# Performance work log

Measured on AMD Instinct MI355X. Metric: run time of the kernel, lower is better.

The kernel has to match this reference:

```python
import jax, jax.numpy as jnp
import numpy as np

B, T, D, L, E = 4096, 4, 1024, 2, 4  # batch, tasks (risk_num+1), dim, layers, experts/task


def setup_inputs() -> dict:
    key = jax.random.key(0)
    ks = jax.random.split(key, 9)
    s = 1.0 / np.sqrt(D).astype(np.float32)  # torch Linear-style uniform scale
    se = 1.0 / np.sqrt(E).astype(np.float32)
    u = lambda k, shape, sc: jax.random.uniform(k, shape, jnp.float32, -sc, sc)
    return {
        "x": jax.random.normal(ks[0], (B, T, D), jnp.float32),
        # per-layer, per-task shared-expert MLP params (mlp_level=2)
        "W1": u(ks[1], (L, T, D, D), s), "b1": u(ks[2], (L, T, D), s),
        "W2": u(ks[3], (L, T, D, D), s), "b2": u(ks[4], (L, T, D), s),
        # integration weights over E (aliased) experts per task
        "inte": u(ks[5], (L, T, E), se),
        # one shared gate per layer: Linear(D -> T) + softmax
        "Wg": u(ks[6], (L, D, T), s), "bg": u(ks[7], (L, T), s),
    }


def reference(x, W1, b1, W2, b2, inte, Wg, bg):
    h = x  # [B, T, D]
    n_layers = W1.shape[0]
    for l in range(n_layers):
        # per-task 2-layer MLP expert (all E experts per task share weights in the
        # original due to [MLP]*E aliasing)
        t1 = jax.nn.relu(jnp.einsum('btd,tdo->bto', h, W1[l]) + b1[l])
        t2 = jax.nn.relu(jnp.einsum('btd,tdo->bto', t1, W2[l]) + b2[l])
        # stack of E identical expert outputs einsum'd with inte weights == scale by sum_e w[t,e]
        teo = t2 * jnp.sum(inte[l], axis=-1)[None, :, None]  # [B, T, D]
        # shared gate applied to each task's output: softmax(Linear(teo)) -> [B, T, T]
        g = jax.nn.softmax(jnp.einsum('btd,dk->btk', teo, Wg[l]) + bg[l], axis=-1)
        # bmm combine + residual
        h = jnp.einsum('btk,bkd->btd', g, teo) + teo
    return h
```

## Files before the change

kernel.cpp:

```cpp
#include <hip/hip_runtime.h>
#include <hip/hip_bf16.h>

#define B_ 4096
#define T_ 4
#define D_ 1024
#define E_ 4

typedef unsigned short ushort_t;
typedef float f32x4 __attribute__((ext_vector_type(4)));
typedef short bf16x8 __attribute__((ext_vector_type(8)));

__device__ __forceinline__ unsigned short f2bf(float f) {
    unsigned int u = __float_as_uint(f);
    u += 0x7FFF + ((u >> 16) & 1);
    return (unsigned short)(u >> 16);
}

__device__ __forceinline__ float bf2f(ushort_t u) {
    return __uint_as_float(((unsigned int)u) << 16);
}

#define GLOBAL_LOAD_LDS16(gp, lp)                                                        \
    __builtin_amdgcn_global_load_lds((const __attribute__((address_space(1))) void*)(gp),\
                                     (__attribute__((address_space(3))) void*)(lp),      \
                                     16, 0, 0)

__global__ __launch_bounds__(256) void k_prep(const float* __restrict__ x,
                                              const float* __restrict__ W1,
                                              const float* __restrict__ W2,
                                              ushort_t* __restrict__ hbf,
                                              ushort_t* __restrict__ W1t,
                                              ushort_t* __restrict__ W2t) {
    const int blk = blockIdx.x;
    const int tid = threadIdx.x;
    if (blk >= 4096) {
        const int base = ((blk - 4096) * 256 + tid) * 8;
        const float4 v0 = *(const float4*)(x + base);
        const float4 v1 = *(const float4*)(x + base + 4);
        bf16x8 o;
        o[0] = (short)f2bf(v0.x); o[1] = (short)f2bf(v0.y);
        o[2] = (short)f2bf(v0.z); o[3] = (short)f2bf(v0.w);
        o[4] = (short)f2bf(v1.x); o[5] = (short)f2bf(v1.y);
        o[6] = (short)f2bf(v1.z); o[7] = (short)f2bf(v1.w);
        const int d = base & (D_ - 1);
        const int t = (base >> 10) & 3;
        const int b = base >> 12;
        *(bf16x8*)(hbf + (size_t)t * B_ * D_ + (size_t)b * D_ + d) = o;
        return;
    }
    const int z = blk >> 8;
    const int ti = blk & 255;
    const int o0 = (ti & 15) * 64, d0 = (ti >> 4) * 64;
    const float* src = (z < 8) ? (W1 + (size_t)z * D_ * D_) : (W2 + (size_t)(z - 8) * D_ * D_);
    ushort_t* dst = (z < 8) ? (W1t + (size_t)z * D_ * D_) : (W2t + (size_t)(z - 8) * D_ * D_);

    __shared__ float tile[64][65];
    const int c4 = tid & 15;
    const int r0 = tid >> 4;
#pragma unroll
    for (int j = 0; j < 4; ++j) {
        const int r = r0 + 16 * j;
        const float4 v = *(const float4*)(src + (size_t)(d0 + r) * D_ + o0 + c4 * 4);
        tile[r][c4 * 4 + 0] = v.x;
        tile[r][c4 * 4 + 1] = v.y;
        tile[r][c4 * 4 + 2] = v.z;
        tile[r][c4 * 4 + 3] = v.w;
    }
    __syncthreads();
    const int cg = tid & 7, ro = tid >> 3;
#pragma unroll
    for (int j = 0; j < 2; ++j) {
        const int o = ro + 32 * j;
        bf16x8 ov;
#pragma unroll
        for (int k = 0; k < 8; ++k) ov[k] = (short)f2bf(tile[cg * 8 + k][o]);
        *(bf16x8*)(dst + (size_t)(o0 + o) * D_ + d0 + cg * 8) = ov;
    }
}

template <bool OUT_BF16>
__global__ __launch_bounds__(512, 2) void k_gemm_bt(
    const ushort_t* __restrict__ A,
    const ushort_t* __restrict__ Bt,
    const float* __restrict__ bias,
    void* __restrict__ out,
    const float* __restrict__ inte)
{
    __shared__ __align__(16) char lds[131072];

    const int f = blockIdx.x;
    const int xcd = f & 7;
    const int tk = xcd >> 1;
    const int ib = f >> 3;
    const int n_blk = ib & 3;
    const int m_blk = ((ib >> 2) << 1) | (xcd & 1);
    const int m0 = m_blk * 256, n0 = n_blk * 256;

    const ushort_t* Ap = A + (size_t)tk * B_ * D_;
    const ushort_t* Bp = Bt + (size_t)tk * D_ * D_;
    const float* bp = bias + tk * D_;

    const int tid = threadIdx.x;
    const int lane = tid & 63, wid = tid >> 6;
    const int lr = lane & 15, quad = lane >> 4;
    const int wmt = (wid & 1) * 128;
    const int wnt = (wid >> 1) * 64;

    const int swz = (lr & 7) << 4;
    const int kk0 = (quad * 16) ^ swz;
    const int kk1 = (64 + quad * 16) ^ swz;

    const int q0 = tid, q1 = tid + 512;
    const ushort_t* gA0 = Ap + (size_t)(m0 + (q0 >> 3)) * D_ + 8 * ((q0 & 7) ^ ((q0 >> 3) & 7));
    const ushort_t* gA1 = Ap + (size_t)(m0 + (q1 >> 3)) * D_ + 8 * ((q1 & 7) ^ ((q1 >> 3) & 7));
    const ushort_t* gB0 = Bp + (size_t)(n0 + (q0 >> 3)) * D_ + 8 * ((q0 & 7) ^ ((q0 >> 3) & 7));
    const ushort_t* gB1 = Bp + (size_t)(n0 + (q1 >> 3)) * D_ + 8 * ((q1 & 7) ^ ((q1 >> 3) & 7));
    char* lA0 = lds + q0 * 16;
    char* lA1 = lds + q1 * 16;
    char* lB0 = lds + 32768 + q0 * 16;
    char* lB1 = lds + 32768 + q1 * 16;

#define STAGE_A(kt, h, s_)                                                     \
    do {                                                                       \
        GLOBAL_LOAD_LDS16(gA0 + (size_t)(h) * 131072 + (kt) * 64,              \
                          lA0 + (s_) * 65536 + (h) * 16384);                   \
        GLOBAL_LOAD_LDS16(gA1 + (size_t)(h) * 131072 + (kt) * 64,              \
                          lA1 + (s_) * 65536 + (h) * 16384);                   \
    } while (0)
#define STAGE_B(kt, h, s_)                                                     \
    do {                                                                       \
        GLOBAL_LOAD_LDS16(gB0 + (size_t)(h) * 131072 + (kt) * 64,              \
                          lB0 + (s_) * 65536 + (h) * 16384);                   \
        GLOBAL_LOAD_LDS16(gB1 + (size_t)(h) * 131072 + (kt) * 64,              \
                          lB1 + (s_) * 65536 + (h) * 16384);                   \
    } while (0)

    f32x4 acc[8][4] = {};

    STAGE_A(0, 0, 0); STAGE_A(0, 1, 0);
    STAGE_B(0, 0, 0); STAGE_B(0, 1, 0);
    STAGE_A(1, 0, 1); STAGE_A(1, 1, 1);
    asm volatile("s_waitcnt vmcnt(4)" ::: "memory");
    __builtin_amdgcn_s_barrier();
    __builtin_amdgcn_sched_barrier(0);

    for (int t = 0; t < 16; ++t) {
        const int s = t & 1;
        const char* As_ = lds + s * 65536;
        const char* Bs_ = lds + s * 65536 + 32768;
        bf16x8 af0[4][2], af1[4][2], bfv[2][2];

#pragma unroll
        for (int mi = 0; mi < 4; ++mi) {
            af0[mi][0] = *(const bf16x8*)(As_ + (wmt + mi * 16 + lr) * 128 + kk0);
            af0[mi][1] = *(const bf16x8*)(As_ + (wmt + mi * 16 + lr) * 128 + kk1);
        }
#pragma unroll
        for (int ni = 0; ni < 2; ++ni) {
            bfv[ni][0] = *(const bf16x8*)(Bs_ + (wnt + ni * 16 + lr) * 128 + kk0);
            bfv[ni][1] = *(const bf16x8*)(Bs_ + (wnt + ni * 16 + lr) * 128 + kk1);
        }
        if (t + 1 < 16) STAGE_B(t + 1, 0, s ^ 1);
        __builtin_amdgcn_s_barrier();
        __builtin_amdgcn_s_setprio(1);
#pragma unroll
        for (int mi = 0; mi < 4; ++mi)
#pragma unroll
            for (int ni = 0; ni < 2; ++ni) {
                acc[mi][ni] = __builtin_amdgcn_mfma_f32_16x16x32_bf16(
                    af0[mi][0], bfv[ni][0], acc[mi][ni], 0, 0, 0);
                acc[mi][ni] = __builtin_amdgcn_mfma_f32_16x16x32_bf16(
                    af0[mi][1], bfv[ni][1], acc[mi][ni], 0, 0, 0);
            }
        __builtin_amdgcn_s_setprio(0);
        __builtin_amdgcn_s_barrier();

#pragma unroll
        for (int mi = 0; mi < 4; ++mi) {
            af1[mi][0] = *(const bf16x8*)(As_ + (wmt + 64 + mi * 16 + lr) * 128 + kk0);
            af1[mi][1] = *(const bf16x8*)(As_ + (wmt + 64 + mi * 16 + lr) * 128 + kk1);
        }
        if (t + 1 < 16) STAGE_B(t + 1, 1, s ^ 1);
        __builtin_amdgcn_s_barrier();
        __builtin_amdgcn_s_setprio(1);
#pragma unroll
        for (int mi = 0; mi < 4; ++mi)
#pragma unroll
            for (int ni = 0; ni < 2; ++ni) {
                acc[4 + mi][ni] = __builtin_amdgcn_mfma_f32_16x16x32_bf16(
                    af1[mi][0], bfv[ni][0], acc[4 + mi][ni], 0, 0, 0);
                acc[4 + mi][ni] = __builtin_amdgcn_mfma_f32_16x16x32_bf16(
                    af1[mi][1], bfv[ni][1], acc[4 + mi][ni], 0, 0, 0);
            }
        __builtin_amdgcn_s_setprio(0);
        __builtin_amdgcn_s_barrier();

#pragma unroll
        for (int ni = 0; ni < 2; ++ni) {
            bfv[ni][0] = *(const bf16x8*)(Bs_ + (wnt + 32 + ni * 16 + lr) * 128 + kk0);
            bfv[ni][1] = *(const bf16x8*)(Bs_ + (wnt + 32 + ni * 16 + lr) * 128 + kk1);
        }
        if (t + 2 < 16) STAGE_A(t + 2, 0, s);
        __builtin_amdgcn_s_barrier();
        __builtin_amdgcn_s_setprio(1);
#pragma unroll
        for (int mi = 0; mi < 4; ++mi)
#pragma unroll
            for (int ni = 0; ni < 2; ++ni) {
                acc[4 + mi][2 + ni] = __builtin_amdgcn_mfma_f32_16x16x32_bf16(
                    af1[mi][0], bfv[ni][0], acc[4 + mi][2 + ni], 0, 0, 0);
                acc[4 + mi][2 + ni] = __builtin_amdgcn_mfma_f32_16x16x32_bf16(
                    af1[mi][1], bfv[ni][1], acc[4 + mi][2 + ni], 0, 0, 0);
            }
        __builtin_amdgcn_s_setprio(0);
        __builtin_amdgcn_s_barrier();

        if (t + 2 < 16) STAGE_A(t + 2, 1, s);
        __builtin_amdgcn_s_barrier();
        __builtin_amdgcn_s_setprio(1);
#pragma unroll
        for (int mi = 0; mi < 4; ++mi)
#pragma unroll
            for (int ni = 0; ni < 2; ++ni) {
                acc[mi][2 + ni] = __builtin_amdgcn_mfma_f32_16x16x32_bf16(
                    af0[mi][0], bfv[ni][0], acc[mi][2 + ni], 0, 0, 0);
                acc[mi][2 + ni] = __builtin_amdgcn_mfma_f32_16x16x32_bf16(
                    af0[mi][1], bfv[ni][1], acc[mi][2 + ni], 0, 0, 0);
            }
        __builtin_amdgcn_s_setprio(0);
        if (t < 14)       asm volatile("s_waitcnt vmcnt(4)" ::: "memory");
        else if (t == 14) asm volatile("s_waitcnt vmcnt(0)" ::: "memory");
        __builtin_amdgcn_s_barrier();
        __builtin_amdgcn_sched_barrier(0);
    }
#undef STAGE_A
#undef STAGE_B

    float scale = 1.0f;
    if (inte) {
        const float* ip = inte + tk * E_;
        scale = ip[0] + ip[1] + ip[2] + ip[3];
    }
#pragma unroll
    for (int mi = 0; mi < 8; ++mi) {
#pragma unroll
        for (int ni = 0; ni < 4; ++ni) {
            const int gcol = n0 + wnt + ni * 16 + lr;
            const float bv = bp[gcol];
#pragma unroll
            for (int r = 0; r < 4; ++r) {
                const int grow = m0 + wmt + mi * 16 + quad * 4 + r;
                float v = acc[mi][ni][r] + bv;
                v = fmaxf(v, 0.0f) * scale;
                const size_t off = (size_t)tk * B_ * D_ + (size_t)grow * D_ + gcol;
                if (OUT_BF16) ((ushort_t*)out)[off] = f2bf(v);
                else          ((float*)out)[off] = v;
            }
        }
    }
}

template <bool FINAL>
__global__ __launch_bounds__(256) void k_gate_combine(
    const ushort_t* __restrict__ teo,
    const float* __restrict__ Wg,
    const float* __restrict__ bg,
    void* __restrict__ out)
{
    const int b = blockIdx.x;
    const int tid = threadIdx.x;
    const int d0 = tid * 4;

    float4 tv[4];
#pragma unroll
    for (int t = 0; t < 4; ++t) {
        const ushort4 r = *(const ushort4*)(teo + (size_t)t * B_ * D_ + (size_t)b * D_ + d0);
        tv[t] = { bf2f(r.x), bf2f(r.y), bf2f(r.z), bf2f(r.w) };
    }
    float4 wg[4];
#pragma unroll
    for (int i = 0; i < 4; ++i)
        wg[i] = *(const float4*)(Wg + (size_t)(d0 + i) * 4);

    float p[16];
#pragma unroll
    for (int t = 0; t < 4; ++t) {
        const float* tvp = (const float*)&tv[t];
#pragma unroll
        for (int k = 0; k < 4; ++k) {
            p[t * 4 + k] = tvp[0] * ((const float*)&wg[0])[k]
                         + tvp[1] * ((const float*)&wg[1])[k]
                         + tvp[2] * ((const float*)&wg[2])[k]
                         + tvp[3] * ((const float*)&wg[3])[k];
        }
    }
#pragma unroll
    for (int i = 0; i < 16; ++i) {
        float v = p[i];
        v += __shfl_xor(v, 1, 64);
        v += __shfl_xor(v, 2, 64);
        v += __shfl_xor(v, 4, 64);
        v += __shfl_xor(v, 8, 64);
        p[i] = v;
    }
    __shared__ float red[16][16];
    __shared__ float fin[16];
    const int grp = tid >> 4;
    if ((tid & 15) == 0) {
#pragma unroll
        for (int i = 0; i < 16; ++i) red[grp][i] = p[i];
    }
    __syncthreads();
    if (tid < 16) {
        float v = 0.0f;
#pragma unroll
        for (int g = 0; g < 16; ++g) v += red[g][tid];
        fin[tid] = v;
    }
    __syncthreads();

    float g[4][4];
#pragma unroll
    for (int t = 0; t < 4; ++t) {
        float lg[4];
#pragma unroll
        for (int k = 0; k < 4; ++k)
            lg[k] = fin[t * 4 + k] + bg[k];
        float mx = fmaxf(fmaxf(lg[0], lg[1]), fmaxf(lg[2], lg[3]));
        float e0 = __expf(lg[0] - mx), e1 = __expf(lg[1] - mx);
        float e2 = __expf(lg[2] - mx), e3 = __expf(lg[3] - mx);
        float inv = 1.0f / (e0 + e1 + e2 + e3);
        g[t][0] = e0 * inv; g[t][1] = e1 * inv; g[t][2] = e2 * inv; g[t][3] = e3 * inv;
    }
#pragma unroll
    for (int t = 0; t < 4; ++t) {
        float o[4];
#pragma unroll
        for (int i = 0; i < 4; ++i) {
            o[i] = g[t][0] * ((const float*)&tv[0])[i]
                 + g[t][1] * ((const float*)&tv[1])[i]
                 + g[t][2] * ((const float*)&tv[2])[i]
                 + g[t][3] * ((const float*)&tv[3])[i]
                 + ((const float*)&tv[t])[i];
        }
        if (FINAL) {
            float4 ov = { o[0], o[1], o[2], o[3] };
            *(float4*)((float*)out + (size_t)b * T_ * D_ + (size_t)t * D_ + d0) = ov;
        } else {
            ushort4 ov = { f2bf(o[0]), f2bf(o[1]), f2bf(o[2]), f2bf(o[3]) };
            *(ushort4*)((ushort_t*)out + (size_t)t * B_ * D_ + (size_t)b * D_ + d0) = ov;
        }
    }
}

extern "C" void kernel_launch(void* const* d_in, const int* in_sizes, int n_in,
                              void* d_out, int out_size, void* d_ws, size_t ws_size,
                              hipStream_t stream) {
    const float* x    = (const float*)d_in[0];
    const float* W1   = (const float*)d_in[1];
    const float* b1   = (const float*)d_in[2];
    const float* W2   = (const float*)d_in[3];
    const float* b2   = (const float*)d_in[4];
    const float* inte = (const float*)d_in[5];
    const float* Wg   = (const float*)d_in[6];
    const float* bg   = (const float*)d_in[7];

    char* ws = (char*)d_ws;
    ushort_t* W1t  = (ushort_t*)(ws);
    ushort_t* W2t  = (ushort_t*)(ws + 33554432);
    ushort_t* Hbf  = (ushort_t*)(ws + 67108864);
    ushort_t* T1bf = (ushort_t*)(ws + 100663296);
    ushort_t* Teo  = (ushort_t*)(ws + 134217728);

    k_prep<<<dim3(12288), 256, 0, stream>>>(x, W1, W2, Hbf, W1t, W2t);

    for (int l = 0; l < 2; ++l) {
        const size_t wOff = (size_t)l * T_ * D_ * D_;
        k_gemm_bt<true><<<dim3(256), 512, 0, stream>>>(Hbf, W1t + wOff, b1 + l * T_ * D_,
                                                       (void*)T1bf, nullptr);
        k_gemm_bt<true><<<dim3(256), 512, 0, stream>>>(T1bf, W2t + wOff, b2 + l * T_ * D_,
                                                       (void*)Teo, inte + l * T_ * E_);
        if (l == 0)
            k_gate_combine<false><<<dim3(B_), 256, 0, stream>>>(
                Teo, Wg + l * D_ * T_, bg + l * T_, (void*)Hbf);
        else
            k_gate_combine<true ><<<dim3(B_), 256, 0, stream>>>(
                Teo, Wg + l * D_ * T_, bg + l * T_, (void*)d_out);
    }
}
```

Before: 349.2 us.

## Fuse per-layer GEMMs and gate-combine into one cooperative persistent kernel

Replaces the six per-layer launches (two GEMMs and one gate-combine per layer) with a single cooperative kernel of 256 blocks. Phases are separated by grid.sync(). The gate-combine phase is rewritten so each 512-thread block handles 16 batch rows in 8 passes of two rows each. This is meant to remove kernel launch gaps and tail effects between stages. In exchange it adds grid-wide barriers and gives the memory-bound gate-combine phase far fewer blocks in flight.

New measurement: 600.5 us. 71.9% more time.

```diff
diff --git a/kernel.cpp b/kernel.cpp
--- a/kernel.cpp
+++ b/kernel.cpp
@@ -1,5 +1,8 @@
 #include <hip/hip_runtime.h>
 #include <hip/hip_bf16.h>
+#include <hip/hip_cooperative_groups.h>
+
+namespace cg = cooperative_groups;
 
 #define B_ 4096
 #define T_ 4
@@ -67,24 +70,22 @@
         tile[r][c4 * 4 + 3] = v.w;
     }
     __syncthreads();
-    const int cg = tid & 7, ro = tid >> 3;
+    const int cg_ = tid & 7, ro = tid >> 3;
 #pragma unroll
     for (int j = 0; j < 2; ++j) {
         const int o = ro + 32 * j;
         bf16x8 ov;
 #pragma unroll
-        for (int k = 0; k < 8; ++k) ov[k] = (short)f2bf(tile[cg * 8 + k][o]);
-        *(bf16x8*)(dst + (size_t)(o0 + o) * D_ + d0 + cg * 8) = ov;
-    }
-}
-
-template <bool OUT_BF16>
-__global__ __launch_bounds__(512, 2) void k_gemm_bt(
-    const ushort_t* __restrict__ A,
-    const ushort_t* __restrict__ Bt,
-    const float* __restrict__ bias,
-    void* __restrict__ out,
-    const float* __restrict__ inte)
+        for (int k = 0; k < 8; ++k) ov[k] = (short)f2bf(tile[cg_ * 8 + k][o]);
+        *(bf16x8*)(dst + (size_t)(o0 + o) * D_ + d0 + cg_ * 8) = ov;
+    }
+}
+
+__device__ void gemm_phase(const ushort_t* __restrict__ A,
+                           const ushort_t* __restrict__ Bt,
+                           const float* __restrict__ bias,
+                           ushort_t* __restrict__ out,
+                           const float* __restrict__ inte)
 {
     __shared__ __align__(16) char lds[131072];
 
@@ -252,105 +253,126 @@
                 const int grow = m0 + wmt + mi * 16 + quad * 4 + r;
                 float v = acc[mi][ni][r] + bv;
                 v = fmaxf(v, 0.0f) * scale;
-                const size_t off = (size_t)tk * B_ * D_ + (size_t)grow * D_ + gcol;
-                if (OUT_BF16) ((ushort_t*)out)[off] = f2bf(v);
-                else          ((float*)out)[off] = v;
-            }
-        }
-    }
-}
-
-template <bool FINAL>
-__global__ __launch_bounds__(256) void k_gate_combine(
-    const ushort_t* __restrict__ teo,
-    const float* __restrict__ Wg,
-    const float* __restrict__ bg,
-    void* __restrict__ out)
+                out[(size_t)tk * B_ * D_ + (size_t)grow * D_ + gcol] = f2bf(v);
+            }
+        }
+    }
+}
+
+__device__ void gc_phase(const ushort_t* __restrict__ teo,
+                         const float* __restrict__ Wg,
+                         const float* __restrict__ bg,
+                         ushort_t* out_bf, float* out_f)
 {
-    const int b = blockIdx.x;
-    const int tid = threadIdx.x;
+    __shared__ float red[2][16][16];
+    __shared__ float fin[2][16];
+    const int half = threadIdx.x >> 8;
+    const int tid = threadIdx.x & 255;
     const int d0 = tid * 4;
 
-    float4 tv[4];
-#pragma unroll
-    for (int t = 0; t < 4; ++t) {
-        const ushort4 r = *(const ushort4*)(teo + (size_t)t * B_ * D_ + (size_t)b * D_ + d0);
-        tv[t] = { bf2f(r.x), bf2f(r.y), bf2f(r.z), bf2f(r.w) };
-    }
-    float4 wg[4];
-#pragma unroll
-    for (int i = 0; i < 4; ++i)
-        wg[i] = *(const float4*)(Wg + (size_t)(d0 + i) * 4);
-
-    float p[16];
-#pragma unroll
-    for (int t = 0; t < 4; ++t) {
-        const float* tvp = (const float*)&tv[t];
-#pragma unroll
-        for (int k = 0; k < 4; ++k) {
-            p[t * 4 + k] = tvp[0] * ((const float*)&wg[0])[k]
-                         + tvp[1] * ((const float*)&wg[1])[k]
-                         + tvp[2] * ((const float*)&wg[2])[k]
-                         + tvp[3] * ((const float*)&wg[3])[k];
-        }
-    }
-#pragma unroll
-    for (int i = 0; i < 16; ++i) {
-        float v = p[i];
-        v += __shfl_xor(v, 1, 64);
-        v += __shfl_xor(v, 2, 64);
-        v += __shfl_xor(v, 4, 64);
-        v += __shfl_xor(v, 8, 64);
-        p[i] = v;
-    }
-    __shared__ float red[16][16];
-    __shared__ float fin[16];
-    const int grp = tid >> 4;
-    if ((tid & 15) == 0) {
-#pragma unroll
-        for (int i = 0; i < 16; ++i) red[grp][i] = p[i];
-    }
-    __syncthreads();
-    if (tid < 16) {
-        float v = 0.0f;
-#pragma unroll
-        for (int g = 0; g < 16; ++g) v += red[g][tid];
-        fin[tid] = v;
-    }
-    __syncthreads();
-
-    float g[4][4];
-#pragma unroll
-    for (int t = 0; t < 4; ++t) {
-        float lg[4];
-#pragma unroll
-        for (int k = 0; k < 4; ++k)
-            lg[k] = fin[t * 4 + k] + bg[k];
-        float mx = fmaxf(fmaxf(lg[0], lg[1]), fmaxf(lg[2], lg[3]));
-        float e0 = __expf(lg[0] - mx), e1 = __expf(lg[1] - mx);
-        float e2 = __expf(lg[2] - mx), e3 = __expf(lg[3] - mx);
-        float inv = 1.0f / (e0 + e1 + e2 + e3);
-        g[t][0] = e0 * inv; g[t][1] = e1 * inv; g[t][2] = e2 * inv; g[t][3] = e3 * inv;
-    }
-#pragma unroll
-    for (int t = 0; t < 4; ++t) {
-        float o[4];
-#pragma unroll
-        for (int i = 0; i < 4; ++i) {
-            o[i] = g[t][0] * ((const float*)&tv[0])[i]
-                 + g[t][1] * ((const float*)&tv[1])[i]
-                 + g[t][2] * ((const float*)&tv[2])[i]
-                 + g[t][3] * ((const float*)&tv[3])[i]
-                 + ((const float*)&tv[t])[i];
-        }
-        if (FINAL) {
-            float4 ov = { o[0], o[1], o[2], o[3] };
-            *(float4*)((float*)out + (size_t)b * T_ * D_ + (size_t)t * D_ + d0) = ov;
-        } else {
-            ushort4 ov = { f2bf(o[0]), f2bf(o[1]), f2bf(o[2]), f2bf(o[3]) };
-            *(ushort4*)((ushort_t*)out + (size_t)t * B_ * D_ + (size_t)b * D_ + d0) = ov;
-        }
-    }
+    for (int pass = 0; pass < 8; ++pass) {
+        const int b = blockIdx.x * 16 + pass * 2 + half;
+
+        float4 tv[4];
+#pragma unroll
+        for (int t = 0; t < 4; ++t) {
+            const ushort4 r = *(const ushort4*)(teo + (size_t)t * B_ * D_ + (size_t)b * D_ + d0);
+            tv[t] = { bf2f(r.x), bf2f(r.y), bf2f(r.z), bf2f(r.w) };
+        }
+        float4 wg[4];
+#pragma unroll
+        for (int i = 0; i < 4; ++i)
+            wg[i] = *(const float4*)(Wg + (size_t)(d0 + i) * 4);
+
+        float p[16];
+#pragma unroll
+        for (int t = 0; t < 4; ++t) {
+            const float* tvp = (const float*)&tv[t];
+#pragma unroll
+            for (int k = 0; k < 4; ++k) {
+                p[t * 4 + k] = tvp[0] * ((const float*)&wg[0])[k]
+                             + tvp[1] * ((const float*)&wg[1])[k]
+                             + tvp[2] * ((const float*)&wg[2])[k]
+                             + tvp[3] * ((const float*)&wg[3])[k];
+            }
+        }
+#pragma unroll
+        for (int i = 0; i < 16; ++i) {
+            float v = p[i];
+            v += __shfl_xor(v, 1, 64);
+            v += __shfl_xor(v, 2, 64);
+            v += __shfl_xor(v, 4, 64);
+            v += __shfl_xor(v, 8, 64);
+            p[i] = v;
+        }
+        const int grp = tid >> 4;
+        if ((tid & 15) == 0) {
+#pragma unroll
+            for (int i = 0; i < 16; ++i) red[half][grp][i] = p[i];
+        }
+        __syncthreads();
+        if (tid < 16) {
+            float v = 0.0f;
+#pragma unroll
+            for (int g = 0; g < 16; ++g) v += red[half][g][tid];
+            fin[half][tid] = v;
+        }
+        __syncthreads();
+
+        float g[4][4];
+#pragma unroll
+        for (int t = 0; t < 4; ++t) {
+            float lg[4];
+#pragma unroll
+            for (int k = 0; k < 4; ++k)
+                lg[k] = fin[half][t * 4 + k] + bg[k];
+            float mx = fmaxf(fmaxf(lg[0], lg[1]), fmaxf(lg[2], lg[3]));
+            float e0 = __expf(lg[0] - mx), e1 = __expf(lg[1] - mx);
+            float e2 = __expf(lg[2] - mx), e3 = __expf(lg[3] - mx);
+            float inv = 1.0f / (e0 + e1 + e2 + e3);
+            g[t][0] = e0 * inv; g[t][1] = e1 * inv; g[t][2] = e2 * inv; g[t][3] = e3 * inv;
+        }
+#pragma unroll
+        for (int t = 0; t < 4; ++t) {
+            float o[4];
+#pragma unroll
+            for (int i = 0; i < 4; ++i) {
+                o[i] = g[t][0] * ((const float*)&tv[0])[i]
+                     + g[t][1] * ((const float*)&tv[1])[i]
+                     + g[t][2] * ((const float*)&tv[2])[i]
+                     + g[t][3] * ((const float*)&tv[3])[i]
+                     + ((const float*)&tv[t])[i];
+            }
+            if (out_f) {
+                float4 ov = { o[0], o[1], o[2], o[3] };
+                *(float4*)(out_f + (size_t)b * T_ * D_ + (size_t)t * D_ + d0) = ov;
+            } else {
+                ushort4 ov = { f2bf(o[0]), f2bf(o[1]), f2bf(o[2]), f2bf(o[3]) };
+                *(ushort4*)(out_bf + (size_t)t * B_ * D_ + (size_t)b * D_ + d0) = ov;
+            }
+        }
+    }
+}
+
+__global__ __launch_bounds__(512, 2) void k_fused(
+    ushort_t* Hbf, ushort_t* T1bf, ushort_t* Teo,
+    const ushort_t* W1t, const ushort_t* W2t,
+    const float* b1, const float* b2, const float* inte,
+    const float* Wg, const float* bg, float* outf)
+{
+    cg::grid_group grid = cg::this_grid();
+
+    gemm_phase(Hbf, W1t, b1, T1bf, nullptr);
+    grid.sync();
+    gemm_phase(T1bf, W2t, b2, Teo, inte);
+    grid.sync();
+    gc_phase(Teo, Wg, bg, Hbf, nullptr);
+    grid.sync();
+    gemm_phase(Hbf, W1t + (size_t)T_ * D_ * D_, b1 + T_ * D_, T1bf, nullptr);
+    grid.sync();
+    gemm_phase(T1bf, W2t + (size_t)T_ * D_ * D_, b2 + T_ * D_, Teo, inte + T_ * E_);
+    grid.sync();
+    gc_phase(Teo, Wg + D_ * T_, bg + T_, nullptr, outf);
 }
 
 extern "C" void kernel_launch(void* const* d_in, const int* in_sizes, int n_in,
@@ -371,20 +393,16 @@
     ushort_t* Hbf  = (ushort_t*)(ws + 67108864);
     ushort_t* T1bf = (ushort_t*)(ws + 100663296);
     ushort_t* Teo  = (ushort_t*)(ws + 134217728);
+    float* outf = (float*)d_out;
 
     k_prep<<<dim3(12288), 256, 0, stream>>>(x, W1, W2, Hbf, W1t, W2t);
 
-    for (int l = 0; l < 2; ++l) {
-        const size_t wOff = (size_t)l * T_ * D_ * D_;
-        k_gemm_bt<true><<<dim3(256), 512, 0, stream>>>(Hbf, W1t + wOff, b1 + l * T_ * D_,
-                                                       (void*)T1bf, nullptr);
-        k_gemm_bt<true><<<dim3(256), 512, 0, stream>>>(T1bf, W2t + wOff, b2 + l * T_ * D_,
-                                                       (void*)Teo, inte + l * T_ * E_);
-        if (l == 0)
-            k_gate_combine<false><<<dim3(B_), 256, 0, stream>>>(
-                Teo, Wg + l * D_ * T_, bg + l * T_, (void*)Hbf);
-        else
-            k_gate_combine<true ><<<dim3(B_), 256, 0, stream>>>(
-                Teo, Wg + l * D_ * T_, bg + l * T_, (void*)d_out);
-    }
-}
+    void* args[] = {
+        (void*)&Hbf, (void*)&T1bf, (void*)&Teo,
+        (void*)&W1t, (void*)&W2t,
+        (void*)&b1, (void*)&b2, (void*)&inte,
+        (void*)&Wg, (void*)&bg, (void*)&outf
+    };
+    hipLaunchCooperativeKernel((const void*)k_fused, dim3(256), dim3(512),
+                               args, 0, stream);
+}
```
